# Optimization experiments

Hardware: AMD Instinct MI355X
Metric: run time of the kernel (lower is better)

The kernel has to match this reference:

```python
import jax, jax.numpy as jnp
import numpy as np

N, E, B = 100000, 1600000, 4
NODE_DIM, EDGE_DIM, H, L, C_DIM = 3, 1, 128, 6, 100


def _mlp2(x, w1, b1, w2, b2):
    # Linear -> ReLU -> Linear
    return jax.nn.relu(x @ w1 + b1) @ w2 + b2


def setup_inputs() -> dict:
    key = jax.random.key(0)
    ks = jax.random.split(key, 32)
    s = 0.02
    inp = {
        "x": jax.random.normal(ks[0], (N, NODE_DIM), jnp.float32),
        "edge_index": jax.random.randint(ks[1], (2, E), 0, N, jnp.int64),
        "edge_attr": jax.random.uniform(ks[2], (E, EDGE_DIM), jnp.float32),
        "t": jax.random.uniform(ks[3], (B,), jnp.float32),
        "batch": jnp.sort(jax.random.randint(ks[4], (N,), 0, B, jnp.int64)),
        "condition": jax.random.normal(ks[5], (B, C_DIM), jnp.float32),
        # input_mlp
        "in_w1": jax.random.normal(ks[6], (NODE_DIM, H), jnp.float32) * s,
        "in_b1": jnp.zeros((H,), jnp.float32),
        "in_w2": jax.random.normal(ks[7], (H, H), jnp.float32) * s,
        "in_b2": jnp.zeros((H,), jnp.float32),
        # time_mlp
        "t_w1": jax.random.normal(ks[8], (1, H), jnp.float32) * s,
        "t_b1": jnp.zeros((H,), jnp.float32),
        "t_w2": jax.random.normal(ks[9], (H, H), jnp.float32) * s,
        "t_b2": jnp.zeros((H,), jnp.float32),
        # condition_mlp
        "c_w1": jax.random.normal(ks[10], (C_DIM, H), jnp.float32) * s,
        "c_b1": jnp.zeros((H,), jnp.float32),
        "c_w2": jax.random.normal(ks[11], (H, H), jnp.float32) * s,
        "c_b2": jnp.zeros((H,), jnp.float32),
        # 6 EdgeConv layers, stacked
        "convW1": jax.random.normal(ks[12], (L, 2 * H + EDGE_DIM, H), jnp.float32) * s,
        "convb1": jnp.zeros((L, H), jnp.float32),
        "convW2": jax.random.normal(ks[13], (L, H, H), jnp.float32) * s,
        "convb2": jnp.zeros((L, H), jnp.float32),
        # output_mlp
        "out_w1": jax.random.normal(ks[14], (H, H), jnp.float32) * s,
        "out_b1": jnp.zeros((H,), jnp.float32),
        "out_w2": jax.random.normal(ks[15], (H, NODE_DIM), jnp.float32) * s,
        "out_b2": jnp.zeros((NODE_DIM,), jnp.float32),
    }
    return inp


def reference(x, edge_index, edge_attr, t, batch, condition,
              in_w1, in_b1, in_w2, in_b2,
              t_w1, t_b1, t_w2, t_b2,
              c_w1, c_b1, c_w2, c_b2,
              convW1, convb1, convW2, convb2,
              out_w1, out_b1, out_w2, out_b2):
    n = x.shape[0]
    b = t.shape[0]
    h = _mlp2(x, in_w1, in_b1, in_w2, in_b2)                       # [N,H]
    time_features = _mlp2(t.reshape(b, 1), t_w1, t_b1, t_w2, t_b2)  # [B,H]
    cond_features = _mlp2(condition, c_w1, c_b1, c_w2, c_b2)        # [B,H]
    h = h + time_features[batch] + cond_features[batch]

    src, dst = edge_index[0], edge_index[1]  # PyG: x_j = x[src], x_i = x[dst]
    # in-degree counts for scatter-mean (zero-degree nodes -> mean = 0)
    cnt = jax.ops.segment_sum(jnp.ones((src.shape[0],), h.dtype), dst, num_segments=n)
    inv_cnt = (1.0 / jnp.maximum(cnt, 1.0))[:, None]               # [N,1]

    for i in range(convW1.shape[0]):
        msg_in = jnp.concatenate([h[dst], h[src], edge_attr], axis=1)  # [E, 2H+1]
        msg = _mlp2(msg_in, convW1[i], convb1[i], convW2[i], convb2[i])  # [E,H]
        agg = jax.ops.segment_sum(msg, dst, num_segments=n) * inv_cnt   # scatter-mean
        h = jax.nn.relu(agg) + h

    return _mlp2(h, out_w1, out_b1, out_w2, out_b2)  # [N, node_dim]
```

## Files before the change

kernel.cpp:

```cpp
#include <hip/hip_runtime.h>
#include <hip/hip_fp16.h>

#define HROW 136

typedef _Float16 h4_t __attribute__((ext_vector_type(4)));
typedef _Float16 h8_t __attribute__((ext_vector_type(8)));
typedef float f32x4_t __attribute__((ext_vector_type(4)));

__global__ void k_tc(const float* __restrict__ t, const float* __restrict__ cond,
                     const float* __restrict__ tw1, const float* __restrict__ tb1,
                     const float* __restrict__ tw2, const float* __restrict__ tb2,
                     const float* __restrict__ cw1, const float* __restrict__ cb1,
                     const float* __restrict__ cw2, const float* __restrict__ cb2,
                     float* __restrict__ tf, float* __restrict__ cf, int B, int CDIM)
{
    __shared__ float hidT[8][128];
    __shared__ float hidC[8][128];
    int j = threadIdx.x;
    for (int b = 0; b < B; ++b) {
        hidT[b][j] = fmaxf(t[b] * tw1[j] + tb1[j], 0.f);
        float s = cb1[j];
        for (int d = 0; d < CDIM; ++d) s += cond[b * CDIM + d] * cw1[d * 128 + j];
        hidC[b][j] = fmaxf(s, 0.f);
    }
    __syncthreads();
    for (int b = 0; b < B; ++b) {
        float s1 = tb2[j], s2 = cb2[j];
        for (int k = 0; k < 128; ++k) {
            s1 += hidT[b][k] * tw2[k * 128 + j];
            s2 += hidC[b][k] * cw2[k * 128 + j];
        }
        tf[b * 128 + j] = s1;
        cf[b * 128 + j] = s2;
    }
}

__global__ void k_prep(const float* __restrict__ convW1, const float* __restrict__ convW2,
                       _Float16* __restrict__ w2t, _Float16* __restrict__ w1at,
                       _Float16* __restrict__ w1bt, int total)
{
    int idx = blockIdx.x * 256 + threadIdx.x;
    if (idx >= total) return;
    int i = idx >> 14;
    int jk = idx & 16383;
    int j = jk >> 7, k = jk & 127;
    w2t[idx]  = (_Float16)convW2[(size_t)i * 16384 + k * 128 + j];
    w1at[idx] = (_Float16)convW1[(size_t)i * 32896 + k * 128 + j];
    w1bt[idx] = (_Float16)convW1[(size_t)i * 32896 + 16384 + k * 128 + j];
}

__global__ void k_prep2(const float* __restrict__ in_w2, const float* __restrict__ out_w1,
                        _Float16* __restrict__ in_w2t, _Float16* __restrict__ ow1t)
{
    int idx = blockIdx.x * 256 + threadIdx.x;
    int which = idx >> 14;
    int jk = idx & 16383;
    int j = jk >> 7, k = jk & 127;
    if (which == 0) in_w2t[jk] = (_Float16)in_w2[k * 128 + j];
    else            ow1t[jk]  = (_Float16)out_w1[k * 128 + j];
}

__global__ void k_count(const int* __restrict__ dst, int* __restrict__ cnt, int E)
{
    int e = blockIdx.x * 256 + threadIdx.x;
    if (e < E) atomicAdd(&cnt[dst[e]], 1);
}

__global__ void k_scan1(const int* __restrict__ cnt, int* __restrict__ bsum, int N)
{
    __shared__ int s[256];
    int i = blockIdx.x * 256 + threadIdx.x;
    int c = (i < N) ? cnt[i] : 0;
    s[threadIdx.x] = (c + 1) & ~1;
    __syncthreads();
    for (int d = 128; d > 0; d >>= 1) {
        if (threadIdx.x < d) s[threadIdx.x] += s[threadIdx.x + d];
        __syncthreads();
    }
    if (threadIdx.x == 0) bsum[blockIdx.x] = s[0];
}

__global__ void k_scan2(const int* __restrict__ bsum, int* __restrict__ boff, int NB)
{
    __shared__ int s[512];
    int t = threadIdx.x;
    int v = (t < NB) ? bsum[t] : 0;
    s[t] = v;
    __syncthreads();
    for (int d = 1; d < 512; d <<= 1) {
        int x = (t >= d) ? s[t - d] : 0;
        __syncthreads();
        s[t] += x;
        __syncthreads();
    }
    if (t < NB) boff[t] = s[t] - v;
}

__global__ void k_scan3(const int* __restrict__ cnt, const int* __restrict__ boff,
                        int* __restrict__ off, int N)
{
    __shared__ int s[256];
    int t = threadIdx.x;
    int i = blockIdx.x * 256 + t;
    int c = (i < N) ? cnt[i] : 0;
    int v = (c + 1) & ~1;
    s[t] = v;
    __syncthreads();
    for (int d = 1; d < 256; d <<= 1) {
        int x = (t >= d) ? s[t - d] : 0;
        __syncthreads();
        s[t] += x;
        __syncthreads();
    }
    if (i < N) off[i] = boff[blockIdx.x] + s[t] - v;
}

__global__ void k_fill(const int* __restrict__ src, const int* __restrict__ dst,
                       const float* __restrict__ ea, const int* __restrict__ off,
                       int* __restrict__ cur, int2* __restrict__ csr, int E)
{
    int e = blockIdx.x * 256 + threadIdx.x;
    if (e < E) {
        int d = dst[e];
        int r = atomicAdd(&cur[d], 1);
        int2 v;
        v.x = src[e];
        v.y = __float_as_int(ea[e]);
        csr[off[d] + r] = v;
    }
}

__device__ __forceinline__ h8_t load_frag(const _Float16* p)
{
    h4_t lo = *(const h4_t*)p;
    h4_t hi = *(const h4_t*)(p + 16);
    h8_t f;
    f[0] = lo[0]; f[1] = lo[1]; f[2] = lo[2]; f[3] = lo[3];
    f[4] = hi[0]; f[5] = hi[1]; f[6] = hi[2]; f[7] = hi[3];
    return f;
}

__device__ __forceinline__ void mfma_gemm64(const _Float16* Al, const _Float16* Wl,
                                            f32x4_t acc[8], int wnt0, int l)
{
    int r16 = l & 15, g4 = (l >> 4) * 4;
    const _Float16* ap = Al + r16 * HROW + g4;
    const _Float16* bp = Wl + (wnt0 * 16 + r16) * HROW + g4;
    #pragma unroll
    for (int ks = 0; ks < 4; ++ks) {
        h8_t b0 = load_frag(bp + ks * 32);
        h8_t b1 = load_frag(bp + 16 * HROW + ks * 32);
        #pragma unroll
        for (int mt = 0; mt < 4; ++mt) {
            h8_t a = load_frag(ap + mt * 16 * HROW + ks * 32);
            acc[mt * 2 + 0] = __builtin_amdgcn_mfma_f32_16x16x32_f16(a, b0, acc[mt * 2 + 0], 0, 0, 0);
            acc[mt * 2 + 1] = __builtin_amdgcn_mfma_f32_16x16x32_f16(a, b1, acc[mt * 2 + 1], 0, 0, 0);
        }
    }
}

__device__ __forceinline__ void stage_w(_Float16* Wl, const _Float16* __restrict__ Wg, int t)
{
    for (int i = t; i < 2048; i += 256) {
        int row = i >> 4, c8 = (i & 15) * 8;
        *(uint4*)&Wl[row * HROW + c8] = *(const uint4*)&Wg[row * 128 + c8];
    }
}

__device__ __forceinline__ void stage_a16(_Float16* Al, const float* __restrict__ g,
                                          int bn0, int N, int t)
{
    for (int i = t; i < 64 * 32; i += 256) {
        int nn = i >> 5, c4 = (i & 31) * 4;
        int n = bn0 + nn;
        float4 v = {0.f, 0.f, 0.f, 0.f};
        if (n < N) v = *(const float4*)&g[(size_t)n * 128 + c4];
        h4_t hv;
        hv[0] = (_Float16)v.x; hv[1] = (_Float16)v.y;
        hv[2] = (_Float16)v.z; hv[3] = (_Float16)v.w;
        *(h4_t*)&Al[nn * HROW + c4] = hv;
    }
}

#define ZERO8(acc) \
    { _Pragma("unroll") for (int z_ = 0; z_ < 8; ++z_) acc[z_] = (f32x4_t){0.f, 0.f, 0.f, 0.f}; }

__global__ __launch_bounds__(256, 3) void k_fused_mfma(
    float* __restrict__ h, const float* S, const int* __restrict__ cnt,
    const _Float16* __restrict__ w2t, const float* __restrict__ b2,
    const _Float16* __restrict__ w1at, const _Float16* __restrict__ w1bt,
    const float* __restrict__ b1n,
    float* P, _Float16* Q, int N)
{
    __shared__ _Float16 Al[64 * HROW];
    __shared__ _Float16 Wl[128 * HROW];
    int bn0 = blockIdx.x * 64;
    int t = threadIdx.x;
    int l = t & 63, wv = t >> 6;
    int wnt0 = wv * 2;
    int r16 = l & 15, g4r = (l >> 4) * 4;

    stage_a16(Al, S, bn0, N, t);
    stage_w(Wl, w2t, t);
    __syncthreads();

    f32x4_t acc[8];
    ZERO8(acc);
    mfma_gemm64(Al, Wl, acc, wnt0, l);

    float hn[8][4];
    #pragma unroll
    for (int q = 0; q < 2; ++q) {
        int j = (wnt0 + q) * 16 + r16;
        float b2v = b2[j];
        #pragma unroll
        for (int mt = 0; mt < 4; ++mt) {
            #pragma unroll
            for (int r = 0; r < 4; ++r) {
                int n = bn0 + mt * 16 + g4r + r;
                float v = 0.f;
                if (n < N) {
                    float agg = acc[mt * 2 + q][r] + b2v;
                    int c = cnt[n];
                    float rr = (c > 0) ? fmaxf(agg, 0.f) : 0.f;
                    v = h[(size_t)n * 128 + j] + rr;
                    h[(size_t)n * 128 + j] = v;
                }
                hn[mt * 2 + q][r] = v;
            }
        }
    }
    __syncthreads();

    #pragma unroll
    for (int q = 0; q < 2; ++q) {
        int j = (wnt0 + q) * 16 + r16;
        #pragma unroll
        for (int mt = 0; mt < 4; ++mt)
            #pragma unroll
            for (int r = 0; r < 4; ++r)
                Al[(mt * 16 + g4r + r) * HROW + j] = (_Float16)hn[mt * 2 + q][r];
    }
    stage_w(Wl, w1at, t);
    __syncthreads();

    ZERO8(acc);
    mfma_gemm64(Al, Wl, acc, wnt0, l);
    #pragma unroll
    for (int q = 0; q < 2; ++q) {
        int j = (wnt0 + q) * 16 + r16;
        float b1v = b1n[j];
        #pragma unroll
        for (int mt = 0; mt < 4; ++mt)
            #pragma unroll
            for (int r = 0; r < 4; ++r) {
                int n = bn0 + mt * 16 + g4r + r;
                if (n < N) P[(size_t)n * 128 + j] = acc[mt * 2 + q][r] + b1v;
            }
    }
    __syncthreads();

    stage_w(Wl, w1bt, t);
    __syncthreads();

    ZERO8(acc);
    mfma_gemm64(Al, Wl, acc, wnt0, l);
    #pragma unroll
    for (int q = 0; q < 2; ++q) {
        int j = (wnt0 + q) * 16 + r16;
        #pragma unroll
        for (int mt = 0; mt < 4; ++mt)
            #pragma unroll
            for (int r = 0; r < 4; ++r) {
                int n = bn0 + mt * 16 + g4r + r;
                if (n < N) Q[(size_t)n * 128 + j] = (_Float16)acc[mt * 2 + q][r];
            }
    }
}

__global__ __launch_bounds__(256, 3) void k_input_pq_mfma(
    const float* __restrict__ x, const int* __restrict__ batch,
    const float* __restrict__ w1, const float* __restrict__ b1,
    const _Float16* __restrict__ in_w2t, const float* __restrict__ b2,
    const float* __restrict__ tf, const float* __restrict__ cf,
    const _Float16* __restrict__ w1at0, const _Float16* __restrict__ w1bt0,
    const float* __restrict__ b1n,
    float* __restrict__ h, float* P, _Float16* Q, int N)
{
    __shared__ _Float16 Al[64 * HROW];
    __shared__ _Float16 Wl[128 * HROW];
    __shared__ float xs[192];
    __shared__ int   bs[64];
    int bn0 = blockIdx.x * 64;
    int t = threadIdx.x;
    int l = t & 63, wv = t >> 6;
    int wnt0 = wv * 2;
    int r16 = l & 15, g4r = (l >> 4) * 4;

    if (t < 192) {
        int nn = t / 3, d = t - nn * 3;
        int n = bn0 + nn;
        xs[t] = (n < N) ? x[(size_t)n * 3 + d] : 0.f;
    }
    if (t < 64) {
        int n = bn0 + t;
        bs[t] = (n < N) ? batch[n] : 0;
    }
    __syncthreads();
    for (int idx = t; idx < 64 * 128; idx += 256) {
        int nn = idx >> 7, k = idx & 127;
        float hid = fmaxf(xs[nn * 3] * w1[k] + xs[nn * 3 + 1] * w1[128 + k]
                          + xs[nn * 3 + 2] * w1[256 + k] + b1[k], 0.f);
        Al[nn * HROW + k] = (_Float16)hid;
    }
    stage_w(Wl, in_w2t, t);
    __syncthreads();

    f32x4_t acc[8];
    ZERO8(acc);
    mfma_gemm64(Al, Wl, acc, wnt0, l);

    float hn[8][4];
    #pragma unroll
    for (int q = 0; q < 2; ++q) {
        int j = (wnt0 + q) * 16 + r16;
        float b2v = b2[j];
        #pragma unroll
        for (int mt = 0; mt < 4; ++mt) {
            #pragma unroll
            for (int r = 0; r < 4; ++r) {
                int nl = mt * 16 + g4r + r;
                int n = bn0 + nl;
                float v = 0.f;
                if (n < N) {
                    int b = bs[nl];
                    v = acc[mt * 2 + q][r] + b2v + tf[b * 128 + j] + cf[b * 128 + j];
                    h[(size_t)n * 128 + j] = v;
                }
                hn[mt * 2 + q][r] = v;
            }
        }
    }
    __syncthreads();

    #pragma unroll
    for (int q = 0; q < 2; ++q) {
        int j = (wnt0 + q) * 16 + r16;
        #pragma unroll
        for (int mt = 0; mt < 4; ++mt)
            #pragma unroll
            for (int r = 0; r < 4; ++r)
                Al[(mt * 16 + g4r + r) * HROW + j] = (_Float16)hn[mt * 2 + q][r];
    }
    stage_w(Wl, w1at0, t);
    __syncthreads();

    ZERO8(acc);
    mfma_gemm64(Al, Wl, acc, wnt0, l);
    #pragma unroll
    for (int q = 0; q < 2; ++q) {
        int j = (wnt0 + q) * 16 + r16;
        float b1v = b1n[j];
        #pragma unroll
        for (int mt = 0; mt < 4; ++mt)
            #pragma unroll
            for (int r = 0; r < 4; ++r) {
                int n = bn0 + mt * 16 + g4r + r;
                if (n < N) P[(size_t)n * 128 + j] = acc[mt * 2 + q][r] + b1v;
            }
    }
    __syncthreads();

    stage_w(Wl, w1bt0, t);
    __syncthreads();

    ZERO8(acc);
    mfma_gemm64(Al, Wl, acc, wnt0, l);
    #pragma unroll
    for (int q = 0; q < 2; ++q) {
        int j = (wnt0 + q) * 16 + r16;
        #pragma unroll
        for (int mt = 0; mt < 4; ++mt)
            #pragma unroll
            for (int r = 0; r < 4; ++r) {
                int n = bn0 + mt * 16 + g4r + r;
                if (n < N) Q[(size_t)n * 128 + j] = (_Float16)acc[mt * 2 + q][r];
            }
    }
}

__global__ __launch_bounds__(256, 3) void k_final_mfma(
    const float* __restrict__ h, const float* S, const int* __restrict__ cnt,
    const _Float16* __restrict__ w2t, const float* __restrict__ b2,
    const _Float16* __restrict__ ow1t, const float* __restrict__ ob1,
    const float* __restrict__ ow2, const float* __restrict__ ob2,
    float* __restrict__ out, int N)
{
    __shared__ _Float16 Al[64 * HROW];
    __shared__ _Float16 Wl[128 * HROW];
    int bn0 = blockIdx.x * 64;
    int t = threadIdx.x;
    int l = t & 63, wv = t >> 6;
    int wnt0 = wv * 2;
    int r16 = l & 15, g4r = (l >> 4) * 4;

    stage_a16(Al, S, bn0, N, t);
    stage_w(Wl, w2t, t);
    __syncthreads();

    f32x4_t acc[8];
    ZERO8(acc);
    mfma_gemm64(Al, Wl, acc, wnt0, l);

    float hn[8][4];
    #pragma unroll
    for (int q = 0; q < 2; ++q) {
        int j = (wnt0 + q) * 16 + r16;
        float b2v = b2[j];
        #pragma unroll
        for (int mt = 0; mt < 4; ++mt) {
            #pragma unroll
            for (int r = 0; r < 4; ++r) {
                int n = bn0 + mt * 16 + g4r + r;
                float v = 0.f;
                if (n < N) {
                    float agg = acc[mt * 2 + q][r] + b2v;
                    int c = cnt[n];
                    float rr = (c > 0) ? fmaxf(agg, 0.f) : 0.f;
                    v = h[(size_t)n * 128 + j] + rr;
                }
                hn[mt * 2 + q][r] = v;
            }
        }
    }
    __syncthreads();

    #pragma unroll
    for (int q = 0; q < 2; ++q) {
        int j = (wnt0 + q) * 16 + r16;
        #pragma unroll
        for (int mt = 0; mt < 4; ++mt)
            #pragma unroll
            for (int r = 0; r < 4; ++r)
                Al[(mt * 16 + g4r + r) * HROW + j] = (_Float16)hn[mt * 2 + q][r];
    }
    stage_w(Wl, ow1t, t);
    __syncthreads();

    ZERO8(acc);
    mfma_gemm64(Al, Wl, acc, wnt0, l);
    __syncthreads();

    #pragma unroll
    for (int q = 0; q < 2; ++q) {
        int j = (wnt0 + q) * 16 + r16;
        float b1v = ob1[j];
        #pragma unroll
        for (int mt = 0; mt < 4; ++mt)
            #pragma unroll
            for (int r = 0; r < 4; ++r)
                Al[(mt * 16 + g4r + r) * HROW + j] = (_Float16)fmaxf(acc[mt * 2 + q][r] + b1v, 0.f);
    }
    __syncthreads();

    if (t < 192) {
        int nn = t / 3, d = t - nn * 3;
        int n = bn0 + nn;
        if (n < N) {
            float s = ob2[d];
            for (int j = 0; j < 128; ++j)
                s += (float)Al[nn * HROW + j] * ow2[j * 3 + d];
            out[(size_t)n * 3 + d] = s;
        }
    }
}

__global__ __launch_bounds__(256) void k_edge(
    float* PS, const __half* __restrict__ Q,
    const int2* __restrict__ csr, const int* __restrict__ off, const int* __restrict__ cnt,
    const float* __restrict__ W1, int N)
{
    int n = blockIdx.x * 4 + (threadIdx.x >> 6);
    int lane = threadIdx.x & 63;
    if (n >= N) return;
    int deg = cnt[n];
    int base = off[n];
    const float* w1c = W1 + 256 * 128;
    float2 p = *(const float2*)&PS[(size_t)n * 128 + lane * 2];
    float2 w = *(const float2*)&w1c[lane * 2];
    const __half* Ql = Q + lane * 2;
    float accx = 0.f, accy = 0.f;
    int e = 0;
    for (; e + 8 <= deg; e += 8) {
        const int4* c4 = (const int4*)(csr + base + e);
        int4 ca = c4[0], cb = c4[1], cc = c4[2], cd = c4[3];
        float2 q0 = __half22float2(*(const __half2*)&Ql[(size_t)ca.x * 128]);
        float2 q1 = __half22float2(*(const __half2*)&Ql[(size_t)ca.z * 128]);
        float2 q2 = __half22float2(*(const __half2*)&Ql[(size_t)cb.x * 128]);
        float2 q3 = __half22float2(*(const __half2*)&Ql[(size_t)cb.z * 128]);
        float2 q4 = __half22float2(*(const __half2*)&Ql[(size_t)cc.x * 128]);
        float2 q5 = __half22float2(*(const __half2*)&Ql[(size_t)cc.z * 128]);
        float2 q6 = __half22float2(*(const __half2*)&Ql[(size_t)cd.x * 128]);
        float2 q7 = __half22float2(*(const __half2*)&Ql[(size_t)cd.z * 128]);
        float e0 = __int_as_float(ca.y), e1 = __int_as_float(ca.w);
        float e2 = __int_as_float(cb.y), e3 = __int_as_float(cb.w);
        float e4 = __int_as_float(cc.y), e5 = __int_as_float(cc.w);
        float e6 = __int_as_float(cd.y), e7 = __int_as_float(cd.w);
        accx += fmaxf(p.x + q0.x + e0 * w.x, 0.f);
        accy += fmaxf(p.y + q0.y + e0 * w.y, 0.f);
        accx += fmaxf(p.x + q1.x + e1 * w.x, 0.f);
        accy += fmaxf(p.y + q1.y + e1 * w.y, 0.f);
        accx += fmaxf(p.x + q2.x + e2 * w.x, 0.f);
        accy += fmaxf(p.y + q2.y + e2 * w.y, 0.f);
        accx += fmaxf(p.x + q3.x + e3 * w.x, 0.f);
        accy += fmaxf(p.y + q3.y + e3 * w.y, 0.f);
        accx += fmaxf(p.x + q4.x + e4 * w.x, 0.f);
        accy += fmaxf(p.y + q4.y + e4 * w.y, 0.f);
        accx += fmaxf(p.x + q5.x + e5 * w.x, 0.f);
        accy += fmaxf(p.y + q5.y + e5 * w.y, 0.f);
        accx += fmaxf(p.x + q6.x + e6 * w.x, 0.f);
        accy += fmaxf(p.y + q6.y + e6 * w.y, 0.f);
        accx += fmaxf(p.x + q7.x + e7 * w.x, 0.f);
        accy += fmaxf(p.y + q7.y + e7 * w.y, 0.f);
    }
    if (e + 4 <= deg) {
        const int4* c4 = (const int4*)(csr + base + e);
        int4 ca = c4[0], cb = c4[1];
        float2 q0 = __half22float2(*(const __half2*)&Ql[(size_t)ca.x * 128]);
        float2 q1 = __half22float2(*(const __half2*)&Ql[(size_t)ca.z * 128]);
        float2 q2 = __half22float2(*(const __half2*)&Ql[(size_t)cb.x * 128]);
        float2 q3 = __half22float2(*(const __half2*)&Ql[(size_t)cb.z * 128]);
        float e0 = __int_as_float(ca.y), e1 = __int_as_float(ca.w);
        float e2 = __int_as_float(cb.y), e3 = __int_as_float(cb.w);
        accx += fmaxf(p.x + q0.x + e0 * w.x, 0.f);
        accy += fmaxf(p.y + q0.y + e0 * w.y, 0.f);
        accx += fmaxf(p.x + q1.x + e1 * w.x, 0.f);
        accy += fmaxf(p.y + q1.y + e1 * w.y, 0.f);
        accx += fmaxf(p.x + q2.x + e2 * w.x, 0.f);
        accy += fmaxf(p.y + q2.y + e2 * w.y, 0.f);
        accx += fmaxf(p.x + q3.x + e3 * w.x, 0.f);
        accy += fmaxf(p.y + q3.y + e3 * w.y, 0.f);
        e += 4;
    }
    if (e + 2 <= deg) {
        const int4* c4 = (const int4*)(csr + base + e);
        int4 ca = c4[0];
        float2 q0 = __half22float2(*(const __half2*)&Ql[(size_t)ca.x * 128]);
        float2 q1 = __half22float2(*(const __half2*)&Ql[(size_t)ca.z * 128]);
        float e0 = __int_as_float(ca.y), e1 = __int_as_float(ca.w);
        accx += fmaxf(p.x + q0.x + e0 * w.x, 0.f);
        accy += fmaxf(p.y + q0.y + e0 * w.y, 0.f);
        accx += fmaxf(p.x + q1.x + e1 * w.x, 0.f);
        accy += fmaxf(p.y + q1.y + e1 * w.y, 0.f);
        e += 2;
    }
    if (e < deg) {
        int2 c = csr[base + e];
        float2 q = __half22float2(*(const __half2*)&Ql[(size_t)c.x * 128]);
        float ec = __int_as_float(c.y);
        accx += fmaxf(p.x + q.x + ec * w.x, 0.f);
        accy += fmaxf(p.y + q.y + ec * w.y, 0.f);
    }
    float invc = 1.f / (float)max(deg, 1);
    float2 o = {accx * invc, accy * invc};
    *(float2*)&PS[(size_t)n * 128 + lane * 2] = o;
}

extern "C" void kernel_launch(void* const* d_in, const int* in_sizes, int n_in,
                              void* d_out, int out_size, void* d_ws, size_t ws_size,
                              hipStream_t stream)
{
    const float* x         = (const float*)d_in[0];
    const int*   edge_idx  = (const int*)d_in[1];
    const float* edge_attr = (const float*)d_in[2];
    const float* tt        = (const float*)d_in[3];
    const int*   batch     = (const int*)d_in[4];
    const float* cond      = (const float*)d_in[5];
    const float* in_w1 = (const float*)d_in[6],  *in_b1 = (const float*)d_in[7];
    const float* in_w2 = (const float*)d_in[8],  *in_b2 = (const float*)d_in[9];
    const float* t_w1  = (const float*)d_in[10], *t_b1  = (const float*)d_in[11];
    const float* t_w2  = (const float*)d_in[12], *t_b2  = (const float*)d_in[13];
    const float* c_w1  = (const float*)d_in[14], *c_b1  = (const float*)d_in[15];
    const float* c_w2  = (const float*)d_in[16], *c_b2  = (const float*)d_in[17];
    const float* convW1 = (const float*)d_in[18], *convb1 = (const float*)d_in[19];
    const float* convW2 = (const float*)d_in[20], *convb2 = (const float*)d_in[21];
    const float* out_w1 = (const float*)d_in[22], *out_b1 = (const float*)d_in[23];
    const float* out_w2 = (const float*)d_in[24], *out_b2 = (const float*)d_in[25];

    const int N = in_sizes[0] / 3;
    const int E = in_sizes[1] / 2;
    const int B = in_sizes[3];
    const int CDIM = in_sizes[5] / B;
    const int L = in_sizes[19] / 128;

    const int* esrc = edge_idx;
    const int* edst = edge_idx + E;

    char* w = (char*)d_ws;
    auto alloc = [&](size_t bytes) -> char* {
        char* p = w;
        w += (bytes + 255) & ~(size_t)255;
        return p;
    };
    float*     h      = (float*)alloc((size_t)N * 128 * 4);
    float*     P      = (float*)alloc((size_t)N * 128 * 4);
    _Float16*  Q      = (_Float16*)alloc((size_t)N * 128 * 2);
    int*       cnt    = (int*)alloc((size_t)N * 4);
    int*       cur    = (int*)alloc((size_t)N * 4);
    int*       off    = (int*)alloc((size_t)N * 4);
    int*       bsum   = (int*)alloc(4096);
    int*       boff   = (int*)alloc(4096);
    int2*      csr    = (int2*)alloc(((size_t)E + N + 8) * 8);
    float*     tf     = (float*)alloc((size_t)B * 128 * 4);
    float*     cf     = (float*)alloc((size_t)B * 128 * 4);
    _Float16*  w2t    = (_Float16*)alloc((size_t)L * 16384 * 2);
    _Float16*  w1at   = (_Float16*)alloc((size_t)L * 16384 * 2);
    _Float16*  w1bt   = (_Float16*)alloc((size_t)L * 16384 * 2);
    _Float16*  in_w2t = (_Float16*)alloc(16384 * 2);
    _Float16*  ow1t   = (_Float16*)alloc(16384 * 2);

    hipMemsetAsync(cnt, 0, (size_t)N * 4, stream);
    hipMemsetAsync(cur, 0, (size_t)N * 4, stream);

    k_tc<<<1, 128, 0, stream>>>(tt, cond, t_w1, t_b1, t_w2, t_b2,
                                c_w1, c_b1, c_w2, c_b2, tf, cf, B, CDIM);

    const int prepTot = L * 16384;
    k_prep<<<(prepTot + 255) / 256, 256, 0, stream>>>(convW1, convW2, w2t, w1at, w1bt, prepTot);
    k_prep2<<<128, 256, 0, stream>>>(in_w2, out_w1, in_w2t, ow1t);

    const int eb = (E + 255) / 256;
    const int nb = (N + 255) / 256;
    k_count<<<eb, 256, 0, stream>>>(edst, cnt, E);
    k_scan1<<<nb, 256, 0, stream>>>(cnt, bsum, N);
    k_scan2<<<1, 512, 0, stream>>>(bsum, boff, nb);
    k_scan3<<<nb, 256, 0, stream>>>(cnt, boff, off, N);
    k_fill<<<eb, 256, 0, stream>>>(esrc, edst, edge_attr, off, cur, csr, E);

    const int gnodes = (N + 63) / 64;
    k_input_pq_mfma<<<gnodes, 256, 0, stream>>>(x, batch, in_w1, in_b1, in_w2t, in_b2,
                                                tf, cf, w1at, w1bt, convb1, h, P, Q, N);

    for (int i = 0; i < L; ++i) {
        const float* b2 = convb2 + (size_t)i * 128;
        k_edge<<<(N + 3) / 4, 256, 0, stream>>>(P, (const __half*)Q, csr, off, cnt,
                                                convW1 + (size_t)i * 257 * 128, N);
        if (i < L - 1) {
            const float* b1n = convb1 + (size_t)(i + 1) * 128;
            k_fused_mfma<<<gnodes, 256, 0, stream>>>(h, P, cnt,
                                                     w2t + (size_t)i * 16384, b2,
                                                     w1at + (size_t)(i + 1) * 16384,
                                                     w1bt + (size_t)(i + 1) * 16384, b1n,
                                                     P, Q, N);
        } else {
            k_final_mfma<<<gnodes, 256, 0, stream>>>(h, P, cnt,
                                                     w2t + (size_t)i * 16384, b2,
                                                     ow1t, out_b1, out_w2, out_b2,
                                                     (float*)d_out, N);
        }
    }
}
```

Baseline: 1.144 ms.

## Fuse edge aggregation into node MLP kernel and store P in fp16

Merges the per-node edge gather/aggregation kernel into the node-level MFMA kernel, so the aggregated mean is written straight into shared memory instead of round-tripping through global P. P is now stored as fp16 and Q is double-buffered, because neighbours of other blocks still read the previous layer's Q while the new one is written. This removes one launch per layer and a large fp32 write and read. The cost is that the gather phase now runs inside a 64-node block at limited occupancy, so latency hiding for the irregular gathers may suffer, and the fp16 P adds rounding.

```diff
diff --git a/kernel.cpp b/kernel.cpp
--- a/kernel.cpp
+++ b/kernel.cpp
@@ -167,328 +167,13 @@
     }
 }
 
-__device__ __forceinline__ void stage_a16(_Float16* Al, const float* __restrict__ g,
-                                          int bn0, int N, int t)
-{
-    for (int i = t; i < 64 * 32; i += 256) {
-        int nn = i >> 5, c4 = (i & 31) * 4;
-        int n = bn0 + nn;
-        float4 v = {0.f, 0.f, 0.f, 0.f};
-        if (n < N) v = *(const float4*)&g[(size_t)n * 128 + c4];
-        h4_t hv;
-        hv[0] = (_Float16)v.x; hv[1] = (_Float16)v.y;
-        hv[2] = (_Float16)v.z; hv[3] = (_Float16)v.w;
-        *(h4_t*)&Al[nn * HROW + c4] = hv;
-    }
-}
-
 #define ZERO8(acc) \
     { _Pragma("unroll") for (int z_ = 0; z_ < 8; ++z_) acc[z_] = (f32x4_t){0.f, 0.f, 0.f, 0.f}; }
 
-__global__ __launch_bounds__(256, 3) void k_fused_mfma(
-    float* __restrict__ h, const float* S, const int* __restrict__ cnt,
-    const _Float16* __restrict__ w2t, const float* __restrict__ b2,
-    const _Float16* __restrict__ w1at, const _Float16* __restrict__ w1bt,
-    const float* __restrict__ b1n,
-    float* P, _Float16* Q, int N)
-{
-    __shared__ _Float16 Al[64 * HROW];
-    __shared__ _Float16 Wl[128 * HROW];
-    int bn0 = blockIdx.x * 64;
-    int t = threadIdx.x;
-    int l = t & 63, wv = t >> 6;
-    int wnt0 = wv * 2;
-    int r16 = l & 15, g4r = (l >> 4) * 4;
-
-    stage_a16(Al, S, bn0, N, t);
-    stage_w(Wl, w2t, t);
-    __syncthreads();
-
-    f32x4_t acc[8];
-    ZERO8(acc);
-    mfma_gemm64(Al, Wl, acc, wnt0, l);
-
-    float hn[8][4];
-    #pragma unroll
-    for (int q = 0; q < 2; ++q) {
-        int j = (wnt0 + q) * 16 + r16;
-        float b2v = b2[j];
-        #pragma unroll
-        for (int mt = 0; mt < 4; ++mt) {
-            #pragma unroll
-            for (int r = 0; r < 4; ++r) {
-                int n = bn0 + mt * 16 + g4r + r;
-                float v = 0.f;
-                if (n < N) {
-                    float agg = acc[mt * 2 + q][r] + b2v;
-                    int c = cnt[n];
-                    float rr = (c > 0) ? fmaxf(agg, 0.f) : 0.f;
-                    v = h[(size_t)n * 128 + j] + rr;
-                    h[(size_t)n * 128 + j] = v;
-                }
-                hn[mt * 2 + q][r] = v;
-            }
-        }
-    }
-    __syncthreads();
-
-    #pragma unroll
-    for (int q = 0; q < 2; ++q) {
-        int j = (wnt0 + q) * 16 + r16;
-        #pragma unroll
-        for (int mt = 0; mt < 4; ++mt)
-            #pragma unroll
-            for (int r = 0; r < 4; ++r)
-                Al[(mt * 16 + g4r + r) * HROW + j] = (_Float16)hn[mt * 2 + q][r];
-    }
-    stage_w(Wl, w1at, t);
-    __syncthreads();
-
-    ZERO8(acc);
-    mfma_gemm64(Al, Wl, acc, wnt0, l);
-    #pragma unroll
-    for (int q = 0; q < 2; ++q) {
-        int j = (wnt0 + q) * 16 + r16;
-        float b1v = b1n[j];
-        #pragma unroll
-        for (int mt = 0; mt < 4; ++mt)
-            #pragma unroll
-            for (int r = 0; r < 4; ++r) {
-                int n = bn0 + mt * 16 + g4r + r;
-                if (n < N) P[(size_t)n * 128 + j] = acc[mt * 2 + q][r] + b1v;
-            }
-    }
-    __syncthreads();
-
-    stage_w(Wl, w1bt, t);
-    __syncthreads();
-
-    ZERO8(acc);
-    mfma_gemm64(Al, Wl, acc, wnt0, l);
-    #pragma unroll
-    for (int q = 0; q < 2; ++q) {
-        int j = (wnt0 + q) * 16 + r16;
-        #pragma unroll
-        for (int mt = 0; mt < 4; ++mt)
-            #pragma unroll
-            for (int r = 0; r < 4; ++r) {
-                int n = bn0 + mt * 16 + g4r + r;
-                if (n < N) Q[(size_t)n * 128 + j] = (_Float16)acc[mt * 2 + q][r];
-            }
-    }
-}
-
-__global__ __launch_bounds__(256, 3) void k_input_pq_mfma(
-    const float* __restrict__ x, const int* __restrict__ batch,
-    const float* __restrict__ w1, const float* __restrict__ b1,
-    const _Float16* __restrict__ in_w2t, const float* __restrict__ b2,
-    const float* __restrict__ tf, const float* __restrict__ cf,
-    const _Float16* __restrict__ w1at0, const _Float16* __restrict__ w1bt0,
-    const float* __restrict__ b1n,
-    float* __restrict__ h, float* P, _Float16* Q, int N)
-{
-    __shared__ _Float16 Al[64 * HROW];
-    __shared__ _Float16 Wl[128 * HROW];
-    __shared__ float xs[192];
-    __shared__ int   bs[64];
-    int bn0 = blockIdx.x * 64;
-    int t = threadIdx.x;
-    int l = t & 63, wv = t >> 6;
-    int wnt0 = wv * 2;
-    int r16 = l & 15, g4r = (l >> 4) * 4;
-
-    if (t < 192) {
-        int nn = t / 3, d = t - nn * 3;
-        int n = bn0 + nn;
-        xs[t] = (n < N) ? x[(size_t)n * 3 + d] : 0.f;
-    }
-    if (t < 64) {
-        int n = bn0 + t;
-        bs[t] = (n < N) ? batch[n] : 0;
-    }
-    __syncthreads();
-    for (int idx = t; idx < 64 * 128; idx += 256) {
-        int nn = idx >> 7, k = idx & 127;
-        float hid = fmaxf(xs[nn * 3] * w1[k] + xs[nn * 3 + 1] * w1[128 + k]
-                          + xs[nn * 3 + 2] * w1[256 + k] + b1[k], 0.f);
-        Al[nn * HROW + k] = (_Float16)hid;
-    }
-    stage_w(Wl, in_w2t, t);
-    __syncthreads();
-
-    f32x4_t acc[8];
-    ZERO8(acc);
-    mfma_gemm64(Al, Wl, acc, wnt0, l);
-
-    float hn[8][4];
-    #pragma unroll
-    for (int q = 0; q < 2; ++q) {
-        int j = (wnt0 + q) * 16 + r16;
-        float b2v = b2[j];
-        #pragma unroll
-        for (int mt = 0; mt < 4; ++mt) {
-            #pragma unroll
-            for (int r = 0; r < 4; ++r) {
-                int nl = mt * 16 + g4r + r;
-                int n = bn0 + nl;
-                float v = 0.f;
-                if (n < N) {
-                    int b = bs[nl];
-                    v = acc[mt * 2 + q][r] + b2v + tf[b * 128 + j] + cf[b * 128 + j];
-                    h[(size_t)n * 128 + j] = v;
-                }
-                hn[mt * 2 + q][r] = v;
-            }
-        }
-    }
-    __syncthreads();
-
-    #pragma unroll
-    for (int q = 0; q < 2; ++q) {
-        int j = (wnt0 + q) * 16 + r16;
-        #pragma unroll
-        for (int mt = 0; mt < 4; ++mt)
-            #pragma unroll
-            for (int r = 0; r < 4; ++r)
-                Al[(mt * 16 + g4r + r) * HROW + j] = (_Float16)hn[mt * 2 + q][r];
-    }
-    stage_w(Wl, w1at0, t);
-    __syncthreads();
-
-    ZERO8(acc);
-    mfma_gemm64(Al, Wl, acc, wnt0, l);
-    #pragma unroll
-    for (int q = 0; q < 2; ++q) {
-        int j = (wnt0 + q) * 16 + r16;
-        float b1v = b1n[j];
-        #pragma unroll
-        for (int mt = 0; mt < 4; ++mt)
-            #pragma unroll
-            for (int r = 0; r < 4; ++r) {
-                int n = bn0 + mt * 16 + g4r + r;
-                if (n < N) P[(size_t)n * 128 + j] = acc[mt * 2 + q][r] + b1v;
-            }
-    }
-    __syncthreads();
-
-    stage_w(Wl, w1bt0, t);
-    __syncthreads();
-
-    ZERO8(acc);
-    mfma_gemm64(Al, Wl, acc, wnt0, l);
-    #pragma unroll
-    for (int q = 0; q < 2; ++q) {
-        int j = (wnt0 + q) * 16 + r16;
-        #pragma unroll
-        for (int mt = 0; mt < 4; ++mt)
-            #pragma unroll
-            for (int r = 0; r < 4; ++r) {
-                int n = bn0 + mt * 16 + g4r + r;
-                if (n < N) Q[(size_t)n * 128 + j] = (_Float16)acc[mt * 2 + q][r];
-            }
-    }
-}
-
-__global__ __launch_bounds__(256, 3) void k_final_mfma(
-    const float* __restrict__ h, const float* S, const int* __restrict__ cnt,
-    const _Float16* __restrict__ w2t, const float* __restrict__ b2,
-    const _Float16* __restrict__ ow1t, const float* __restrict__ ob1,
-    const float* __restrict__ ow2, const float* __restrict__ ob2,
-    float* __restrict__ out, int N)
-{
-    __shared__ _Float16 Al[64 * HROW];
-    __shared__ _Float16 Wl[128 * HROW];
-    int bn0 = blockIdx.x * 64;
-    int t = threadIdx.x;
-    int l = t & 63, wv = t >> 6;
-    int wnt0 = wv * 2;
-    int r16 = l & 15, g4r = (l >> 4) * 4;
-
-    stage_a16(Al, S, bn0, N, t);
-    stage_w(Wl, w2t, t);
-    __syncthreads();
-
-    f32x4_t acc[8];
-    ZERO8(acc);
-    mfma_gemm64(Al, Wl, acc, wnt0, l);
-
-    float hn[8][4];
-    #pragma unroll
-    for (int q = 0; q < 2; ++q) {
-        int j = (wnt0 + q) * 16 + r16;
-        float b2v = b2[j];
-        #pragma unroll
-        for (int mt = 0; mt < 4; ++mt) {
-            #pragma unroll
-            for (int r = 0; r < 4; ++r) {
-                int n = bn0 + mt * 16 + g4r + r;
-                float v = 0.f;
-                if (n < N) {
-                    float agg = acc[mt * 2 + q][r] + b2v;
-                    int c = cnt[n];
-                    float rr = (c > 0) ? fmaxf(agg, 0.f) : 0.f;
-                    v = h[(size_t)n * 128 + j] + rr;
-                }
-                hn[mt * 2 + q][r] = v;
-            }
-        }
-    }
-    __syncthreads();
-
-    #pragma unroll
-    for (int q = 0; q < 2; ++q) {
-        int j = (wnt0 + q) * 16 + r16;
-        #pragma unroll
-        for (int mt = 0; mt < 4; ++mt)
-            #pragma unroll
-            for (int r = 0; r < 4; ++r)
-                Al[(mt * 16 + g4r + r) * HROW + j] = (_Float16)hn[mt * 2 + q][r];
-    }
-    stage_w(Wl, ow1t, t);
-    __syncthreads();
-
-    ZERO8(acc);
-    mfma_gemm64(Al, Wl, acc, wnt0, l);
-    __syncthreads();
-
-    #pragma unroll
-    for (int q = 0; q < 2; ++q) {
-        int j = (wnt0 + q) * 16 + r16;
-        float b1v = ob1[j];
-        #pragma unroll
-        for (int mt = 0; mt < 4; ++mt)
-            #pragma unroll
-            for (int r = 0; r < 4; ++r)
-                Al[(mt * 16 + g4r + r) * HROW + j] = (_Float16)fmaxf(acc[mt * 2 + q][r] + b1v, 0.f);
-    }
-    __syncthreads();
-
-    if (t < 192) {
-        int nn = t / 3, d = t - nn * 3;
-        int n = bn0 + nn;
-        if (n < N) {
-            float s = ob2[d];
-            for (int j = 0; j < 128; ++j)
-                s += (float)Al[nn * HROW + j] * ow2[j * 3 + d];
-            out[(size_t)n * 3 + d] = s;
-        }
-    }
-}
-
-__global__ __launch_bounds__(256) void k_edge(
-    float* PS, const __half* __restrict__ Q,
-    const int2* __restrict__ csr, const int* __restrict__ off, const int* __restrict__ cnt,
-    const float* __restrict__ W1, int N)
-{
-    int n = blockIdx.x * 4 + (threadIdx.x >> 6);
-    int lane = threadIdx.x & 63;
-    if (n >= N) return;
-    int deg = cnt[n];
-    int base = off[n];
-    const float* w1c = W1 + 256 * 128;
-    float2 p = *(const float2*)&PS[(size_t)n * 128 + lane * 2];
-    float2 w = *(const float2*)&w1c[lane * 2];
-    const __half* Ql = Q + lane * 2;
+__device__ __forceinline__ float2 agg_node(const __half* __restrict__ Ql,
+                                           const int2* __restrict__ csr,
+                                           int base, int deg, float2 p, float2 w)
+{
     float accx = 0.f, accy = 0.f;
     int e = 0;
     for (; e + 8 <= deg; e += 8) {
@@ -561,9 +246,339 @@
         accx += fmaxf(p.x + q.x + ec * w.x, 0.f);
         accy += fmaxf(p.y + q.y + ec * w.y, 0.f);
     }
-    float invc = 1.f / (float)max(deg, 1);
-    float2 o = {accx * invc, accy * invc};
-    *(float2*)&PS[(size_t)n * 128 + lane * 2] = o;
+    return {accx, accy};
+}
+
+__global__ __launch_bounds__(256, 3) void k_conv(
+    float* __restrict__ h, _Float16* __restrict__ P ,
+    const int* __restrict__ cnt, const int* __restrict__ off,
+    const int2* __restrict__ csr, const _Float16* __restrict__ Qin,
+    const float* __restrict__ w1c,
+    const _Float16* __restrict__ w2t, const float* __restrict__ b2,
+    const _Float16* __restrict__ w1at, const _Float16* __restrict__ w1bt,
+    const float* __restrict__ b1n,
+    _Float16* __restrict__ Qout, int N)
+{
+    __shared__ _Float16 Al[64 * HROW];
+    __shared__ _Float16 Wl[128 * HROW];
+    int bn0 = blockIdx.x * 64;
+    int t = threadIdx.x;
+    int l = t & 63, wv = t >> 6;
+    int wnt0 = wv * 2;
+    int r16 = l & 15, g4r = (l >> 4) * 4;
+
+    {
+        float2 wch = *(const float2*)&w1c[l * 2];
+        const __half* Ql = (const __half*)Qin + l * 2;
+        #pragma unroll 1
+        for (int s_ = 0; s_ < 16; ++s_) {
+            int nl = wv * 16 + s_;
+            int n = bn0 + nl;
+            float2 sv = {0.f, 0.f};
+            if (n < N) {
+                int deg = cnt[n];
+                int base = off[n];
+                float2 p = __half22float2(*(const __half2*)&P[(size_t)n * 128 + l * 2]);
+                sv = agg_node(Ql, csr, base, deg, p, wch);
+                float invc = 1.f / (float)max(deg, 1);
+                sv.x *= invc; sv.y *= invc;
+            }
+            *(__half2*)&Al[nl * HROW + l * 2] = __floats2half2_rn(sv.x, sv.y);
+        }
+    }
+    stage_w(Wl, w2t, t);
+    __syncthreads();
+
+    f32x4_t acc[8];
+    ZERO8(acc);
+    mfma_gemm64(Al, Wl, acc, wnt0, l);
+
+    float hn[8][4];
+    #pragma unroll
+    for (int q = 0; q < 2; ++q) {
+        int j = (wnt0 + q) * 16 + r16;
+        float b2v = b2[j];
+        #pragma unroll
+        for (int mt = 0; mt < 4; ++mt) {
+            #pragma unroll
+            for (int r = 0; r < 4; ++r) {
+                int n = bn0 + mt * 16 + g4r + r;
+                float v = 0.f;
+                if (n < N) {
+                    float agg = acc[mt * 2 + q][r] + b2v;
+                    int c = cnt[n];
+                    float rr = (c > 0) ? fmaxf(agg, 0.f) : 0.f;
+                    v = h[(size_t)n * 128 + j] + rr;
+                    h[(size_t)n * 128 + j] = v;
+                }
+                hn[mt * 2 + q][r] = v;
+            }
+        }
+    }
+    __syncthreads();
+
+    #pragma unroll
+    for (int q = 0; q < 2; ++q) {
+        int j = (wnt0 + q) * 16 + r16;
+        #pragma unroll
+        for (int mt = 0; mt < 4; ++mt)
+            #pragma unroll
+            for (int r = 0; r < 4; ++r)
+                Al[(mt * 16 + g4r + r) * HROW + j] = (_Float16)hn[mt * 2 + q][r];
+    }
+    stage_w(Wl, w1at, t);
+    __syncthreads();
+
+    ZERO8(acc);
+    mfma_gemm64(Al, Wl, acc, wnt0, l);
+    #pragma unroll
+    for (int q = 0; q < 2; ++q) {
+        int j = (wnt0 + q) * 16 + r16;
+        float b1v = b1n[j];
+        #pragma unroll
+        for (int mt = 0; mt < 4; ++mt)
+            #pragma unroll
+            for (int r = 0; r < 4; ++r) {
+                int n = bn0 + mt * 16 + g4r + r;
+                if (n < N) P[(size_t)n * 128 + j] = (_Float16)(acc[mt * 2 + q][r] + b1v);
+            }
+    }
+    __syncthreads();
+
+    stage_w(Wl, w1bt, t);
+    __syncthreads();
+
+    ZERO8(acc);
+    mfma_gemm64(Al, Wl, acc, wnt0, l);
+    #pragma unroll
+    for (int q = 0; q < 2; ++q) {
+        int j = (wnt0 + q) * 16 + r16;
+        #pragma unroll
+        for (int mt = 0; mt < 4; ++mt)
+            #pragma unroll
+            for (int r = 0; r < 4; ++r) {
+                int n = bn0 + mt * 16 + g4r + r;
+                if (n < N) Qout[(size_t)n * 128 + j] = (_Float16)acc[mt * 2 + q][r];
+            }
+    }
+}
+
+__global__ __launch_bounds__(256, 3) void k_conv_final(
+    const float* __restrict__ h, const _Float16* __restrict__ P,
+    const int* __restrict__ cnt, const int* __restrict__ off,
+    const int2* __restrict__ csr, const _Float16* __restrict__ Qin,
+    const float* __restrict__ w1c,
+    const _Float16* __restrict__ w2t, const float* __restrict__ b2,
+    const _Float16* __restrict__ ow1t, const float* __restrict__ ob1,
+    const float* __restrict__ ow2, const float* __restrict__ ob2,
+    float* __restrict__ out, int N)
+{
+    __shared__ _Float16 Al[64 * HROW];
+    __shared__ _Float16 Wl[128 * HROW];
+    int bn0 = blockIdx.x * 64;
+    int t = threadIdx.x;
+    int l = t & 63, wv = t >> 6;
+    int wnt0 = wv * 2;
+    int r16 = l & 15, g4r = (l >> 4) * 4;
+
+    {
+        float2 wch = *(const float2*)&w1c[l * 2];
+        const __half* Ql = (const __half*)Qin + l * 2;
+        #pragma unroll 1
+        for (int s_ = 0; s_ < 16; ++s_) {
+            int nl = wv * 16 + s_;
+            int n = bn0 + nl;
+            float2 sv = {0.f, 0.f};
+            if (n < N) {
+                int deg = cnt[n];
+                int base = off[n];
+                float2 p = __half22float2(*(const __half2*)&P[(size_t)n * 128 + l * 2]);
+                sv = agg_node(Ql, csr, base, deg, p, wch);
+                float invc = 1.f / (float)max(deg, 1);
+                sv.x *= invc; sv.y *= invc;
+            }
+            *(__half2*)&Al[nl * HROW + l * 2] = __floats2half2_rn(sv.x, sv.y);
+        }
+    }
+    stage_w(Wl, w2t, t);
+    __syncthreads();
+
+    f32x4_t acc[8];
+    ZERO8(acc);
+    mfma_gemm64(Al, Wl, acc, wnt0, l);
+
+    float hn[8][4];
+    #pragma unroll
+    for (int q = 0; q < 2; ++q) {
+        int j = (wnt0 + q) * 16 + r16;
+        float b2v = b2[j];
+        #pragma unroll
+        for (int mt = 0; mt < 4; ++mt) {
+            #pragma unroll
+            for (int r = 0; r < 4; ++r) {
+                int n = bn0 + mt * 16 + g4r + r;
+                float v = 0.f;
+                if (n < N) {
+                    float agg = acc[mt * 2 + q][r] + b2v;
+                    int c = cnt[n];
+                    float rr = (c > 0) ? fmaxf(agg, 0.f) : 0.f;
+                    v = h[(size_t)n * 128 + j] + rr;
+                }
+                hn[mt * 2 + q][r] = v;
+            }
+        }
+    }
+    __syncthreads();
+
+    #pragma unroll
+    for (int q = 0; q < 2; ++q) {
+        int j = (wnt0 + q) * 16 + r16;
+        #pragma unroll
+        for (int mt = 0; mt < 4; ++mt)
+            #pragma unroll
+            for (int r = 0; r < 4; ++r)
+                Al[(mt * 16 + g4r + r) * HROW + j] = (_Float16)hn[mt * 2 + q][r];
+    }
+    stage_w(Wl, ow1t, t);
+    __syncthreads();
+
+    ZERO8(acc);
+    mfma_gemm64(Al, Wl, acc, wnt0, l);
+    __syncthreads();
+
+    #pragma unroll
+    for (int q = 0; q < 2; ++q) {
+        int j = (wnt0 + q) * 16 + r16;
+        float b1v = ob1[j];
+        #pragma unroll
+        for (int mt = 0; mt < 4; ++mt)
+            #pragma unroll
+            for (int r = 0; r < 4; ++r)
+                Al[(mt * 16 + g4r + r) * HROW + j] = (_Float16)fmaxf(acc[mt * 2 + q][r] + b1v, 0.f);
+    }
+    __syncthreads();
+
+    if (t < 192) {
+        int nn = t / 3, d = t - nn * 3;
+        int n = bn0 + nn;
+        if (n < N) {
+            float s = ob2[d];
+            for (int j = 0; j < 128; ++j)
+                s += (float)Al[nn * HROW + j] * ow2[j * 3 + d];
+            out[(size_t)n * 3 + d] = s;
+        }
+    }
+}
+
+__global__ __launch_bounds__(256, 3) void k_input_pq_mfma(
+    const float* __restrict__ x, const int* __restrict__ batch,
+    const float* __restrict__ w1, const float* __restrict__ b1,
+    const _Float16* __restrict__ in_w2t, const float* __restrict__ b2,
+    const float* __restrict__ tf, const float* __restrict__ cf,
+    const _Float16* __restrict__ w1at0, const _Float16* __restrict__ w1bt0,
+    const float* __restrict__ b1n,
+    float* __restrict__ h, _Float16* __restrict__ P, _Float16* __restrict__ Q, int N)
+{
+    __shared__ _Float16 Al[64 * HROW];
+    __shared__ _Float16 Wl[128 * HROW];
+    __shared__ float xs[192];
+    __shared__ int   bs[64];
+    int bn0 = blockIdx.x * 64;
+    int t = threadIdx.x;
+    int l = t & 63, wv = t >> 6;
+    int wnt0 = wv * 2;
+    int r16 = l & 15, g4r = (l >> 4) * 4;
+
+    if (t < 192) {
+        int nn = t / 3, d = t - nn * 3;
+        int n = bn0 + nn;
+        xs[t] = (n < N) ? x[(size_t)n * 3 + d] : 0.f;
+    }
+    if (t < 64) {
+        int n = bn0 + t;
+        bs[t] = (n < N) ? batch[n] : 0;
+    }
+    __syncthreads();
+    for (int idx = t; idx < 64 * 128; idx += 256) {
+        int nn = idx >> 7, k = idx & 127;
+        float hid = fmaxf(xs[nn * 3] * w1[k] + xs[nn * 3 + 1] * w1[128 + k]
+                          + xs[nn * 3 + 2] * w1[256 + k] + b1[k], 0.f);
+        Al[nn * HROW + k] = (_Float16)hid;
+    }
+    stage_w(Wl, in_w2t, t);
+    __syncthreads();
+
+    f32x4_t acc[8];
+    ZERO8(acc);
+    mfma_gemm64(Al, Wl, acc, wnt0, l);
+
+    float hn[8][4];
+    #pragma unroll
+    for (int q = 0; q < 2; ++q) {
+        int j = (wnt0 + q) * 16 + r16;
+        float b2v = b2[j];
+        #pragma unroll
+        for (int mt = 0; mt < 4; ++mt) {
+            #pragma unroll
+            for (int r = 0; r < 4; ++r) {
+                int nl = mt * 16 + g4r + r;
+                int n = bn0 + nl;
+                float v = 0.f;
+                if (n < N) {
+                    int b = bs[nl];
+                    v = acc[mt * 2 + q][r] + b2v + tf[b * 128 + j] + cf[b * 128 + j];
+                    h[(size_t)n * 128 + j] = v;
+                }
+                hn[mt * 2 + q][r] = v;
+            }
+        }
+    }
+    __syncthreads();
+
+    #pragma unroll
+    for (int q = 0; q < 2; ++q) {
+        int j = (wnt0 + q) * 16 + r16;
+        #pragma unroll
+        for (int mt = 0; mt < 4; ++mt)
+            #pragma unroll
+            for (int r = 0; r < 4; ++r)
+                Al[(mt * 16 + g4r + r) * HROW + j] = (_Float16)hn[mt * 2 + q][r];
+    }
+    stage_w(Wl, w1at0, t);
+    __syncthreads();
+
+    ZERO8(acc);
+    mfma_gemm64(Al, Wl, acc, wnt0, l);
+    #pragma unroll
+    for (int q = 0; q < 2; ++q) {
+        int j = (wnt0 + q) * 16 + r16;
+        float b1v = b1n[j];
+        #pragma unroll
+        for (int mt = 0; mt < 4; ++mt)
+            #pragma unroll
+            for (int r = 0; r < 4; ++r) {
+                int n = bn0 + mt * 16 + g4r + r;
+                if (n < N) P[(size_t)n * 128 + j] = (_Float16)(acc[mt * 2 + q][r] + b1v);
+            }
+    }
+    __syncthreads();
+
+    stage_w(Wl, w1bt0, t);
+    __syncthreads();
+
+    ZERO8(acc);
+    mfma_gemm64(Al, Wl, acc, wnt0, l);
+    #pragma unroll
+    for (int q = 0; q < 2; ++q) {
+        int j = (wnt0 + q) * 16 + r16;
+        #pragma unroll
+        for (int mt = 0; mt < 4; ++mt)
+            #pragma unroll
+            for (int r = 0; r < 4; ++r) {
+                int n = bn0 + mt * 16 + g4r + r;
+                if (n < N) Q[(size_t)n * 128 + j] = (_Float16)acc[mt * 2 + q][r];
+            }
+    }
 }
 
 extern "C" void kernel_launch(void* const* d_in, const int* in_sizes, int n_in,
@@ -603,8 +618,9 @@
         return p;
     };
     float*     h      = (float*)alloc((size_t)N * 128 * 4);
-    float*     P      = (float*)alloc((size_t)N * 128 * 4);
-    _Float16*  Q      = (_Float16*)alloc((size_t)N * 128 * 2);
+    _Float16*  Pp     = (_Float16*)alloc((size_t)N * 128 * 2);
+    _Float16*  Qa     = (_Float16*)alloc((size_t)N * 128 * 2);
+    _Float16*  Qb     = (_Float16*)alloc((size_t)N * 128 * 2);
     int*       cnt    = (int*)alloc((size_t)N * 4);
     int*       cur    = (int*)alloc((size_t)N * 4);
     int*       off    = (int*)alloc((size_t)N * 4);
@@ -619,6 +635,8 @@
     _Float16*  in_w2t = (_Float16*)alloc(16384 * 2);
     _Float16*  ow1t   = (_Float16*)alloc(16384 * 2);
 
+    _Float16* Qbuf[2] = {Qa, Qb};
+
     hipMemsetAsync(cnt, 0, (size_t)N * 4, stream);
     hipMemsetAsync(cur, 0, (size_t)N * 4, stream);
 
@@ -639,21 +657,20 @@
 
     const int gnodes = (N + 63) / 64;
     k_input_pq_mfma<<<gnodes, 256, 0, stream>>>(x, batch, in_w1, in_b1, in_w2t, in_b2,
-                                                tf, cf, w1at, w1bt, convb1, h, P, Q, N);
+                                                tf, cf, w1at, w1bt, convb1, h, Pp, Qa, N);
 
     for (int i = 0; i < L; ++i) {
-        const float* b2 = convb2 + (size_t)i * 128;
-        k_edge<<<(N + 3) / 4, 256, 0, stream>>>(P, (const __half*)Q, csr, off, cnt,
-                                                convW1 + (size_t)i * 257 * 128, N);
+        const float* w1c = convW1 + (size_t)i * 257 * 128 + 256 * 128;
+        const float* b2  = convb2 + (size_t)i * 128;
         if (i < L - 1) {
             const float* b1n = convb1 + (size_t)(i + 1) * 128;
-            k_fused_mfma<<<gnodes, 256, 0, stream>>>(h, P, cnt,
-                                                     w2t + (size_t)i * 16384, b2,
-                                                     w1at + (size_t)(i + 1) * 16384,
-                                                     w1bt + (size_t)(i + 1) * 16384, b1n,
-                                                     P, Q, N);
+            k_conv<<<gnodes, 256, 0, stream>>>(h, Pp, cnt, off, csr, Qbuf[i & 1], w1c,
+                                               w2t + (size_t)i * 16384, b2,
+                                               w1at + (size_t)(i + 1) * 16384,
+                                               w1bt + (size_t)(i + 1) * 16384, b1n,
+                                               Qbuf[(i + 1) & 1], N);
         } else {
-            k_final_mfma<<<gnodes, 256, 0, stream>>>(h, P, cnt,
+            k_conv_final<<<gnodes, 256, 0, stream>>>(h, Pp, cnt, off, csr, Qbuf[i & 1], w1c,
                                                      w2t + (size_t)i * 16384, b2,
                                                      ow1t, out_b1, out_w2, out_b2,
                                                      (float*)d_out, N);
```

Result: slower. 1.439 ms (+25.7%).
